# Kernel tuning notes

Measured on AMD Instinct MI355X. Metric: run time of the kernel, lower is better.

## Reference

```python
import jax, jax.numpy as jnp
import numpy as np

NUM_HEADS = 8
WS = 8          # window_size
MO = 12         # (1 + overlap) * window_size
PAD = 2         # overlap * window_size / 2


def setup_inputs() -> dict:
    key = jax.random.key(0)
    ks = jax.random.split(key, 5)
    B, C, H, W = 16, 256, 64, 64
    x = jax.random.normal(ks[0], (B, C, H, W), jnp.float32)
    W1 = jax.random.normal(ks[1], (3 * C, C), jnp.float32) * 0.02
    b1 = jnp.zeros((3 * C,), jnp.float32)
    W2 = jax.random.normal(ks[2], (C, C), jnp.float32) * 0.02
    b2 = jnp.zeros((C,), jnp.float32)
    return {"x": x, "W1": W1, "b1": b1, "W2": W2, "b2": b2}


def _unfold_windows(t, nwin):
    # t: (B, H, W, C) -> overlapping windows (B, nH, nwin, nwin, MO*MO, E)
    # Matches torch nn.Unfold(kernel=MO, stride=WS, padding=PAD) layout:
    # channels outermost, then kernel rows, then kernel cols.
    B, H, W, C = t.shape
    E = C // NUM_HEADS
    p = jnp.pad(t.transpose(0, 3, 1, 2), ((0, 0), (0, 0), (PAD, PAD), (PAD, PAD)))
    idx = (jnp.arange(nwin) * WS)[:, None] + jnp.arange(MO)  # (nwin, MO)
    g = p[:, :, idx]            # (B, C, nwin, MO, Wp)
    g = g[:, :, :, :, idx]      # (B, C, nwin, MO, nwin, MO)
    g = g.transpose(0, 1, 2, 4, 3, 5)            # (B, C, nwin, nwin, MO, MO)
    g = g.reshape(B, NUM_HEADS, E, nwin, nwin, MO * MO)
    return g.transpose(0, 1, 3, 4, 5, 2)         # (B, nH, nwin, nwin, MO^2, E)


def reference(x, W1, b1, W2, b2):
    B, C, H, W = x.shape
    E = C // NUM_HEADS
    nwin = H // WS
    t = x.transpose(0, 2, 3, 1)                  # (B, H, W, C)
    qkv = t @ W1.T + b1                          # (B, H, W, 3C)
    # '(c K)' layout with K=3: channel index outer, K inner -> strided split
    Q = qkv[..., 0::3]
    K = qkv[..., 1::3]
    V = qkv[..., 2::3]
    # Q -> non-overlapping windows: (B, nH, nwin, nwin, WS^2, E)
    Qw = Q.reshape(B, nwin, WS, nwin, WS, NUM_HEADS, E)
    Qw = Qw.transpose(0, 5, 1, 3, 2, 4, 6).reshape(B, NUM_HEADS, nwin, nwin, WS * WS, E)
    Kw = _unfold_windows(K, nwin)
    Vw = _unfold_windows(V, nwin)
    scale = 1.0 / jnp.sqrt(jnp.float32(E))
    scores = jnp.einsum('bhijqe,bhijke->bhijqk', Qw, Kw) * scale  # (B,nH,nw,nw,WS^2,MO^2)
    A = jax.nn.softmax(scores, axis=-1)
    out = jnp.einsum('bhijqk,bhijke->bhijqe', A, Vw)              # (B,nH,nw,nw,WS^2,E)
    out = out.reshape(B, NUM_HEADS, nwin, nwin, WS, WS, E)
    out = out.transpose(0, 2, 4, 3, 5, 1, 6).reshape(B, H, W, C)
    y = out @ W2.T + b2                                           # (B, H, W, C)
    return y.transpose(0, 3, 1, 2)                                # (B, C, H, W)
```

## Files before the change

### kernel.cpp

```cpp
#include <hip/hip_runtime.h>
#include <stdint.h>

typedef unsigned short u16;
typedef unsigned int   u32;
typedef __bf16 bf16x8_t __attribute__((ext_vector_type(8)));
typedef float  f32x4_t  __attribute__((ext_vector_type(4)));

#define MFMA16(a, b, c) __builtin_amdgcn_mfma_f32_16x16x32_bf16((a), (b), (c), 0, 0, 0)

__device__ __forceinline__ float bf2f(u16 u) {
    union { u32 i; float f; } c; c.i = ((u32)u) << 16; return c.f;
}
__device__ __forceinline__ u16 f2bf(float f) {
    union { float f; u32 i; } c; c.f = f;
    u32 x = c.i;
    return (u16)((x + 0x7fffu + ((x >> 16) & 1u)) >> 16);
}

typedef const unsigned int __attribute__((address_space(1)))* gas_t;
typedef unsigned int __attribute__((address_space(3)))* las_t;
__device__ __forceinline__ void gload16(const u16* g, const u16* l) {
    __builtin_amdgcn_global_load_lds((gas_t)(const void*)g, (las_t)(void*)l, 16, 0, 0);
}

__device__ __forceinline__ u32 detect_fp32(const u16* __restrict__ xu,
                                           int tid, int* wcnt) {
    u16 w = xu[2 * tid];
    int e = (w >> 7) & 0xff;
    int ok = (e >= 80 && e <= 160) ? 1 : 0;
    unsigned long long m = __ballot(ok);
    if ((tid & 63) == 0) wcnt[tid >> 6] = __popcll(m);
    __syncthreads();
    int cnt = wcnt[0] + wcnt[1] + wcnt[2] + wcnt[3];
    return (cnt < 160) ? 1u : 0u;
}

__global__ __launch_bounds__(256) void conv_w(const u16* __restrict__ xu,
                                              const void* __restrict__ W1,
                                              const void* __restrict__ b1,
                                              const void* __restrict__ W2,
                                              const void* __restrict__ b2,
                                              u16* __restrict__ W1b,
                                              u16* __restrict__ b1b,
                                              u16* __restrict__ W2b,
                                              u16* __restrict__ b2b) {
    __shared__ int wcnt[4];
    u32 f = detect_fp32(xu, threadIdx.x, wcnt);
    int i = blockIdx.x * 256 + threadIdx.x;
    const int n1 = 196608, n2 = 768, n3 = 65536;
    const void* src; u16* dst; int li;
    if (i < n1)                { src = W1; dst = W1b; li = i; }
    else if (i < n1 + n2)      { src = b1; dst = b1b; li = i - n1; }
    else if (i < n1 + n2 + n3) { src = W2; dst = W2b; li = i - n1 - n2; }
    else                       { src = b2; dst = b2b; li = i - n1 - n2 - n3; }
    u16 v;
    if (f) v = f2bf(((const float*)src)[li]);
    else   v = ((const u16*)src)[li];
    dst[li] = v;
}

__global__ __launch_bounds__(256) void conv_x(const void* __restrict__ X,
                                              u16* __restrict__ XT) {
    __shared__ __align__(16) u16 tile[64][68];
    __shared__ int wcnt[4];
    const int tid = threadIdx.x;
    u32 f = detect_fp32((const u16*)X, tid, wcnt);
    const int b = blockIdx.z, c0 = blockIdx.y * 64, h0 = blockIdx.x * 64;
    const int col = tid & 63, rq = tid >> 6;
    if (f) {
        const float* Xf = (const float*)X;
#pragma unroll
        for (int i = 0; i < 16; i++) {
            int row = i * 4 + rq;
            tile[row][col] = f2bf(Xf[((size_t)(b * 256 + c0 + row)) * 4096 + h0 + col]);
        }
    } else {
        const u16* Xh = (const u16*)X;
#pragma unroll
        for (int i = 0; i < 16; i++) {
            int row = i * 4 + rq;
            tile[row][col] = Xh[((size_t)(b * 256 + c0 + row)) * 4096 + h0 + col];
        }
    }
    __syncthreads();
#pragma unroll
    for (int i = 0; i < 16; i++) {
        int row = i * 4 + rq;
        XT[((size_t)(b * 4096 + h0 + row)) * 256 + c0 + col] = tile[col][row];
    }
}

__global__ __launch_bounds__(256) void gemm_qkv(const u16* __restrict__ XT,
                                                const u16* __restrict__ W1,
                                                const u16* __restrict__ b1,
                                                u16* __restrict__ Q2,
                                                u16* __restrict__ K2,
                                                u16* __restrict__ V2) {
    __shared__ __align__(16) u16 smem[128 * 64 + 96 * 64];
    u16* sA = smem;
    u16* sB = smem + 128 * 64;
    u16* Cs = smem;

    const int tid  = threadIdx.x;
    const int lane = tid & 63, wave = tid >> 6;
    const int quad = lane >> 4, l16 = lane & 15;
    const int wm = wave * 32;
    const int bx = blockIdx.x;
    const int bm = (bx >> 6) * 8 + (bx & 7);
    const int h  = (bx >> 3) & 7;
    const int o_base = h * 96;

    f32x4_t acc[2][6];
    const f32x4_t zz = {0.f, 0.f, 0.f, 0.f};
#pragma unroll
    for (int i = 0; i < 2; i++)
#pragma unroll
        for (int j = 0; j < 6; j++) acc[i][j] = zz;

    const int sub = lane >> 3;
    const int cpw = (lane & 7) ^ sub;
    const u16* gA[4]; const u16* gB[3];
    const u16* lA[4]; const u16* lB[3];
#pragma unroll
    for (int i = 0; i < 4; i++) {
        int r8 = (wave * 4 + i) * 8;
        gA[i] = XT + ((size_t)(bm * 128 + r8 + sub)) * 256 + cpw * 8;
        lA[i] = sA + r8 * 64;
    }
#pragma unroll
    for (int i = 0; i < 3; i++) {
        int r8 = (wave * 3 + i) * 8;
        gB[i] = W1 + ((size_t)(o_base + r8 + sub)) * 256 + cpw * 8;
        lB[i] = sB + r8 * 64;
    }

    for (int kt = 0; kt < 256; kt += 64) {
        __syncthreads();
#pragma unroll
        for (int i = 0; i < 4; i++) gload16(gA[i] + kt, lA[i]);
#pragma unroll
        for (int i = 0; i < 3; i++) gload16(gB[i] + kt, lB[i]);
        __syncthreads();
#pragma unroll
        for (int ks = 0; ks < 2; ks++) {
            bf16x8_t af[2], bg[6];
#pragma unroll
            for (int i = 0; i < 2; i++) {
                int row = wm + i * 16 + l16;
                int cp = (ks * 4 + quad) ^ (row & 7);
                af[i] = *(const bf16x8_t*)(sA + row * 64 + cp * 8);
            }
#pragma unroll
            for (int j = 0; j < 6; j++) {
                int row = j * 16 + l16;
                int cp = (ks * 4 + quad) ^ (row & 7);
                bg[j] = *(const bf16x8_t*)(sB + row * 64 + cp * 8);
            }
#pragma unroll
            for (int i = 0; i < 2; i++)
#pragma unroll
                for (int j = 0; j < 6; j++)
                    acc[i][j] = MFMA16(af[i], bg[j], acc[i][j]);
        }
    }

    __syncthreads();
#pragma unroll
    for (int j = 0; j < 6; j++) {
        float bias = bf2f(b1[o_base + j * 16 + l16]);
#pragma unroll
        for (int i = 0; i < 2; i++) {
            int m = wm + i * 16 + quad * 4;
#pragma unroll
            for (int r = 0; r < 4; r++)
                Cs[(m + r) * 104 + j * 16 + l16] = f2bf(acc[i][j][r] + bias);
        }
    }
    __syncthreads();

    const int b = bm >> 5;
    const int hw0 = (bm & 31) * 128;
    const size_t hb = ((size_t)(b * 8 + h)) * 4096;
#pragma unroll
    for (int it = 0; it < 2; it++) {
        int u = it * 256 + tid;
        int px = u >> 2, ch = u & 3;
        size_t gaddr = (hb + hw0 + px) * 32 + ch * 8;
#pragma unroll
        for (int w = 0; w < 3; w++) {
            u16 vals[8];
#pragma unroll
            for (int jj = 0; jj < 8; jj++)
                vals[jj] = Cs[px * 104 + 3 * (ch * 8 + jj) + w];
            uint4 pk;
            pk.x = (u32)vals[0] | ((u32)vals[1] << 16);
            pk.y = (u32)vals[2] | ((u32)vals[3] << 16);
            pk.z = (u32)vals[4] | ((u32)vals[5] << 16);
            pk.w = (u32)vals[6] | ((u32)vals[7] << 16);
            u16* dst = (w == 0) ? Q2 : (w == 1) ? K2 : V2;
            *(uint4*)(dst + gaddr) = pk;
        }
    }
}

__global__ __launch_bounds__(256) void attn_kernel(const u16* __restrict__ Q2,
                                                   const u16* __restrict__ K2,
                                                   const u16* __restrict__ V2,
                                                   u16* __restrict__ Op) {
    __shared__ __align__(16) u16 smem[16128];
    u16* Ks = smem;
    u16* Ps = smem;
    u16* Vt = smem + 10752;

    const int tid  = threadIdx.x;
    const int lane = tid & 63, wave = tid >> 6;
    const int quad = lane >> 4, l16 = lane & 15;
    const int win = blockIdx.x, head = blockIdx.y, b = blockIdx.z;
    const int wi = win >> 3, wj = win & 7;
    const size_t hb = ((size_t)(b * 8 + head)) * 4096;

    bf16x8_t aF;
    {
        int px = wave * 16 + l16;
        int qy = px >> 3, qx = px & 7;
        aF = *(const bf16x8_t*)(Q2 + (hb + (wi * 8 + qy) * 64 + wj * 8 + qx) * 32 + quad * 8);
    }
    for (int u = tid; u < 576; u += 256) {
        int px = u >> 2, ch = u & 3;
        int py = px / 12, kx = px - py * 12;
        int gy = wi * 8 - 2 + py, gx = wj * 8 - 2 + kx;
        uint4 kv = make_uint4(0, 0, 0, 0), vv = make_uint4(0, 0, 0, 0);
        if (gy >= 0 && gy < 64 && gx >= 0 && gx < 64) {
            size_t off = (hb + gy * 64 + gx) * 32 + ch * 8;
            kv = *(const uint4*)(K2 + off);
            vv = *(const uint4*)(V2 + off);
        }
        *(uint4*)(Ks + px * 40 + ch * 8) = kv;
        int colp = px ^ (ch << 3);
        int e0 = ch * 8;
        u32 w0[4] = {vv.x, vv.y, vv.z, vv.w};
#pragma unroll
        for (int p = 0; p < 4; p++) {
            Vt[(e0 + 2 * p    ) * 168 + colp] = (u16)(w0[p] & 0xffff);
            Vt[(e0 + 2 * p + 1) * 168 + colp] = (u16)(w0[p] >> 16);
        }
    }
    for (int t = tid; t < 512; t += 256) {
        int e = t >> 4, cl = 144 + (t & 15);
        Vt[e * 168 + (cl ^ ((e >> 3) << 3))] = 0;
    }
    __syncthreads();

    float s[9][4];
    {
        const f32x4_t zz = {0.f, 0.f, 0.f, 0.f};
#pragma unroll
        for (int j = 0; j < 9; j++) {
            bf16x8_t bF = *(const bf16x8_t*)(Ks + (j * 16 + l16) * 40 + quad * 8);
            f32x4_t d = MFMA16(aF, bF, zz);
#pragma unroll
            for (int r = 0; r < 4; r++) s[j][r] = d[r];
        }
    }
    float mx[4] = {-1e30f, -1e30f, -1e30f, -1e30f};
#pragma unroll
    for (int j = 0; j < 9; j++)
#pragma unroll
        for (int r = 0; r < 4; r++) mx[r] = fmaxf(mx[r], s[j][r]);
#pragma unroll
    for (int off = 1; off < 16; off <<= 1)
#pragma unroll
        for (int r = 0; r < 4; r++) mx[r] = fmaxf(mx[r], __shfl_xor(mx[r], off, 16));

    __syncthreads();

    *(unsigned long long*)(Ps + (wave * 16 + l16) * 168 + 144 + quad * 4) = 0ULL;

    const float scale = 0.17677669529663687f;
    float msc[4];
#pragma unroll
    for (int r = 0; r < 4; r++) msc[r] = mx[r] * scale;
    float sm[4] = {0.f, 0.f, 0.f, 0.f};
#pragma unroll
    for (int j = 0; j < 9; j++) {
#pragma unroll
        for (int r = 0; r < 4; r++) {
            float p = __expf(fmaf(s[j][r], scale, -msc[r]));
            sm[r] += p;
            Ps[(wave * 16 + quad * 4 + r) * 168 + j * 16 + l16] = f2bf(p);
        }
    }
#pragma unroll
    for (int off = 1; off < 16; off <<= 1)
#pragma unroll
        for (int r = 0; r < 4; r++) sm[r] += __shfl_xor(sm[r], off, 16);

    __syncthreads();

    f32x4_t oa[2];
    oa[0] = (f32x4_t){0.f, 0.f, 0.f, 0.f};
    oa[1] = (f32x4_t){0.f, 0.f, 0.f, 0.f};
#pragma unroll
    for (int kk = 0; kk < 5; kk++) {
        bf16x8_t aP = *(const bf16x8_t*)(Ps + (wave * 16 + l16) * 168 + kk * 32 + quad * 8);
#pragma unroll
        for (int nt = 0; nt < 2; nt++) {
            int er = nt * 16 + l16;
            int sw = (er >> 3) << 3;
            bf16x8_t bV = *(const bf16x8_t*)(Vt + er * 168 + ((kk * 32 + quad * 8) ^ sw));
            oa[nt] = MFMA16(aP, bV, oa[nt]);
        }
    }
    float inv[4];
#pragma unroll
    for (int r = 0; r < 4; r++) inv[r] = 1.0f / sm[r];
#pragma unroll
    for (int nt = 0; nt < 2; nt++) {
        int e = nt * 16 + l16;
#pragma unroll
        for (int r = 0; r < 4; r++) {
            int q = wave * 16 + quad * 4 + r;
            int qy = q >> 3, qx = q & 7;
            size_t pix = (size_t)(b * 4096) + (wi * 8 + qy) * 64 + (wj * 8 + qx);
            Op[pix * 256 + head * 32 + e] = f2bf(oa[nt][r] * inv[r]);
        }
    }
}

__device__ __forceinline__ void gemm_loop(const u16* __restrict__ A,
                                          const u16* __restrict__ B,
                                          int K, int bm, int bn,
                                          u16* sA, u16* sB, f32x4_t acc[4][4]) {
    const int tid  = threadIdx.x;
    const int lane = tid & 63, wave = tid >> 6;
    const int quad = lane >> 4, l16 = lane & 15;
    const int wm = (wave >> 1) * 64, wn = (wave & 1) * 64;

    const int sub = lane >> 3;
    const int cpw = (lane & 7) ^ sub;
    const u16* gA[4]; const u16* gB[4];
    const u16* lA[4]; const u16* lB[4];
#pragma unroll
    for (int i = 0; i < 4; i++) {
        int r8 = (wave * 4 + i) * 8;
        gA[i] = A + ((size_t)(bm * 128 + r8 + sub)) * K + cpw * 8;
        gB[i] = B + ((size_t)(bn * 128 + r8 + sub)) * K + cpw * 8;
        lA[i] = sA + r8 * 64;
        lB[i] = sB + r8 * 64;
    }

    for (int kt = 0; kt < K; kt += 64) {
        __syncthreads();
#pragma unroll
        for (int i = 0; i < 4; i++) gload16(gA[i] + kt, lA[i]);
#pragma unroll
        for (int i = 0; i < 4; i++) gload16(gB[i] + kt, lB[i]);
        __syncthreads();
#pragma unroll
        for (int ks = 0; ks < 2; ks++) {
            bf16x8_t af[4], bg[4];
#pragma unroll
            for (int i = 0; i < 4; i++) {
                int row = wm + i * 16 + l16;
                int cp = (ks * 4 + quad) ^ (row & 7);
                af[i] = *(const bf16x8_t*)(sA + row * 64 + cp * 8);
            }
#pragma unroll
            for (int j = 0; j < 4; j++) {
                int row = wn + j * 16 + l16;
                int cp = (ks * 4 + quad) ^ (row & 7);
                bg[j] = *(const bf16x8_t*)(sB + row * 64 + cp * 8);
            }
#pragma unroll
            for (int i = 0; i < 4; i++)
#pragma unroll
                for (int j = 0; j < 4; j++)
                    acc[i][j] = MFMA16(af[i], bg[j], acc[i][j]);
        }
    }
}

__global__ __launch_bounds__(256) void gemm_out(const u16* __restrict__ xu,
                                                const u16* __restrict__ Ap,
                                                const u16* __restrict__ W2,
                                                const u16* __restrict__ b2,
                                                void* __restrict__ Y) {
    __shared__ __align__(16) u16 sA[128 * 64];
    __shared__ __align__(16) u16 sB[128 * 64];
    __shared__ int wcnt[4];
    const u32 out_f32 = detect_fp32(xu, threadIdx.x, wcnt);

    f32x4_t acc[4][4];
    const f32x4_t zz = {0.f, 0.f, 0.f, 0.f};
#pragma unroll
    for (int i = 0; i < 4; i++)
#pragma unroll
        for (int j = 0; j < 4; j++) acc[i][j] = zz;

    const int bm = blockIdx.x, bn = blockIdx.y;
    gemm_loop(Ap, W2, 256, bm, bn, sA, sB, acc);

    const int lane = threadIdx.x & 63, wave = threadIdx.x >> 6;
    const int quad = lane >> 4, l16 = lane & 15;
    const int wm = (wave >> 1) * 64, wn = (wave & 1) * 64;
    const int b = bm >> 5;
    const int hw0 = (bm & 31) * 128;
#pragma unroll
    for (int j = 0; j < 4; j++) {
        int o = bn * 128 + wn + j * 16 + l16;
        float bias = bf2f(b2[o]);
        size_t base = ((size_t)(b * 256 + o)) * 4096;
        if (out_f32) {
            float* Yf = (float*)Y;
#pragma unroll
            for (int i = 0; i < 4; i++) {
                int m0 = hw0 + wm + i * 16 + quad * 4;
                f32x4_t ov;
#pragma unroll
                for (int r = 0; r < 4; r++) ov[r] = acc[i][j][r] + bias;
                *(f32x4_t*)(Yf + base + m0) = ov;
            }
        } else {
            u16* Yh = (u16*)Y;
#pragma unroll
            for (int i = 0; i < 4; i++) {
                int m0 = hw0 + wm + i * 16 + quad * 4;
                u32 lo = (u32)f2bf(acc[i][j][0] + bias) | ((u32)f2bf(acc[i][j][1] + bias) << 16);
                u32 hi = (u32)f2bf(acc[i][j][2] + bias) | ((u32)f2bf(acc[i][j][3] + bias) << 16);
                u32* d32 = (u32*)(Yh + base + m0);
                d32[0] = lo; d32[1] = hi;
            }
        }
    }
}

extern "C" void kernel_launch(void* const* d_in, const int* in_sizes, int n_in,
                              void* d_out, int out_size, void* d_ws, size_t ws_size,
                              hipStream_t stream) {
    (void)in_sizes; (void)n_in; (void)out_size; (void)ws_size;
    const void* x  = d_in[0];
    const void* W1 = d_in[1];
    const void* b1 = d_in[2];
    const void* W2 = d_in[3];
    const void* b2 = d_in[4];
    const u16* xu = (const u16*)x;

    char* ws = (char*)d_ws;
    const size_t MB32 = (size_t)32 * 1024 * 1024;
    u16* xT  = (u16*)(ws);
    u16* Q2  = (u16*)(ws + MB32);
    u16* K2  = (u16*)(ws + 2 * MB32);
    u16* V2  = (u16*)(ws + 3 * MB32);
    u16* W1b = (u16*)(ws + 4 * MB32);
    u16* b1b = W1b + 196608;
    u16* W2b = b1b + 768;
    u16* b2b = W2b + 65536;
    u16* Op  = xT;

    conv_w  <<<1028, 256, 0, stream>>>(xu, W1, b1, W2, b2, W1b, b1b, W2b, b2b);
    conv_x  <<<dim3(64, 4, 16), 256, 0, stream>>>(x, xT);
    gemm_qkv<<<4096, 256, 0, stream>>>(xT, W1b, b1b, Q2, K2, V2);
    attn_kernel<<<dim3(64, 8, 16), 256, 0, stream>>>(Q2, K2, V2, Op);
    gemm_out<<<dim3(512, 2), 256, 0, stream>>>(xu, Op, W2b, b2b, d_out);
}
```

Before: 244.0 us.

## Permute W1 rows so QKV epilogue writes contiguous vectors; split K/V loads

```diff
diff --git a/kernel.cpp b/kernel.cpp
--- a/kernel.cpp
+++ b/kernel.cpp
@@ -48,15 +48,25 @@
     u32 f = detect_fp32(xu, threadIdx.x, wcnt);
     int i = blockIdx.x * 256 + threadIdx.x;
     const int n1 = 196608, n2 = 768, n3 = 65536;
-    const void* src; u16* dst; int li;
-    if (i < n1)                { src = W1; dst = W1b; li = i; }
-    else if (i < n1 + n2)      { src = b1; dst = b1b; li = i - n1; }
-    else if (i < n1 + n2 + n3) { src = W2; dst = W2b; li = i - n1 - n2; }
-    else                       { src = b2; dst = b2b; li = i - n1 - n2 - n3; }
-    u16 v;
-    if (f) v = f2bf(((const float*)src)[li]);
-    else   v = ((const u16*)src)[li];
-    dst[li] = v;
+    if (i < n1) {
+        int o = i >> 8, col = i & 255;
+        int h = o / 96, rem = o - h * 96;
+        int w = rem >> 5, e = rem & 31;
+        int src = (3 * (h * 32 + e) + w) * 256 + col;
+        W1b[i] = f ? f2bf(((const float*)W1)[src]) : ((const u16*)W1)[src];
+    } else if (i < n1 + n2) {
+        int o = i - n1;
+        int h = o / 96, rem = o - h * 96;
+        int w = rem >> 5, e = rem & 31;
+        int src = 3 * (h * 32 + e) + w;
+        b1b[o] = f ? f2bf(((const float*)b1)[src]) : ((const u16*)b1)[src];
+    } else if (i < n1 + n2 + n3) {
+        int li = i - n1 - n2;
+        W2b[li] = f ? f2bf(((const float*)W2)[li]) : ((const u16*)W2)[li];
+    } else {
+        int li = i - n1 - n2 - n3;
+        b2b[li] = f ? f2bf(((const float*)b2)[li]) : ((const u16*)b2)[li];
+    }
 }
 
 __global__ __launch_bounds__(256) void conv_x(const void* __restrict__ X,
@@ -186,20 +196,9 @@
         int u = it * 256 + tid;
         int px = u >> 2, ch = u & 3;
         size_t gaddr = (hb + hw0 + px) * 32 + ch * 8;
-#pragma unroll
-        for (int w = 0; w < 3; w++) {
-            u16 vals[8];
-#pragma unroll
-            for (int jj = 0; jj < 8; jj++)
-                vals[jj] = Cs[px * 104 + 3 * (ch * 8 + jj) + w];
-            uint4 pk;
-            pk.x = (u32)vals[0] | ((u32)vals[1] << 16);
-            pk.y = (u32)vals[2] | ((u32)vals[3] << 16);
-            pk.z = (u32)vals[4] | ((u32)vals[5] << 16);
-            pk.w = (u32)vals[6] | ((u32)vals[7] << 16);
-            u16* dst = (w == 0) ? Q2 : (w == 1) ? K2 : V2;
-            *(uint4*)(dst + gaddr) = pk;
-        }
+        *(uint4*)(Q2 + gaddr) = *(const uint4*)(Cs + px * 104 +      ch * 8);
+        *(uint4*)(K2 + gaddr) = *(const uint4*)(Cs + px * 104 + 32 + ch * 8);
+        *(uint4*)(V2 + gaddr) = *(const uint4*)(Cs + px * 104 + 64 + ch * 8);
     }
 }
 
@@ -229,13 +228,18 @@
         int px = u >> 2, ch = u & 3;
         int py = px / 12, kx = px - py * 12;
         int gy = wi * 8 - 2 + py, gx = wj * 8 - 2 + kx;
-        uint4 kv = make_uint4(0, 0, 0, 0), vv = make_uint4(0, 0, 0, 0);
-        if (gy >= 0 && gy < 64 && gx >= 0 && gx < 64) {
-            size_t off = (hb + gy * 64 + gx) * 32 + ch * 8;
-            kv = *(const uint4*)(K2 + off);
-            vv = *(const uint4*)(V2 + off);
-        }
+        uint4 kv = make_uint4(0, 0, 0, 0);
+        if (gy >= 0 && gy < 64 && gx >= 0 && gx < 64)
+            kv = *(const uint4*)(K2 + (hb + gy * 64 + gx) * 32 + ch * 8);
         *(uint4*)(Ks + px * 40 + ch * 8) = kv;
+    }
+    for (int u = tid; u < 576; u += 256) {
+        int ch = u / 144, px = u - ch * 144;
+        int py = px / 12, kx = px - py * 12;
+        int gy = wi * 8 - 2 + py, gx = wj * 8 - 2 + kx;
+        uint4 vv = make_uint4(0, 0, 0, 0);
+        if (gy >= 0 && gy < 64 && gx >= 0 && gx < 64)
+            vv = *(const uint4*)(V2 + (hb + gy * 64 + gx) * 32 + ch * 8);
         int colp = px ^ (ch << 3);
         int e0 = ch * 8;
         u32 w0[4] = {vv.x, vv.y, vv.z, vv.w};
```

Measured after the change: 237.9 us. 2.5% less time.
